# Kernel optimization log

Hardware: AMD Instinct MI355X
Metric: run time of the kernel (lower is better)

## Reference

```python
import jax, jax.numpy as jnp
import numpy as np

NUM_MID = 10   # hard-coded num_mid_nodes in HiPool.__init__
NUM_HIGH = 5   # ceil(10 / 2)


def map_low_to_high(num_low, num_high):
    # eye(num_high) repeat_interleaved by ceil(low/high) rows, truncated to num_low
    # == one-hot of i // edges_per_high
    edges_per_high = -(-num_low // num_high)
    return jax.nn.one_hot(jnp.arange(num_low) // edges_per_high, num_high,
                          dtype=jnp.float32)  # [low, high]


def cluster_attention(x, mapping, att):
    # x: [s, d], mapping: [s, m], att: [d, d]
    mid = mapping.T @ x                              # [m, d]
    scores = (mid @ att) @ x.T                       # [m, s]
    scores = scores * (1.0 - mapping).T              # zero (not -inf) own-cluster entries, as in source
    scores = jax.nn.softmax(scores, axis=1)
    return scores @ x + mid                          # [m, d]


def dense_gcn(x, adj, W, b):
    # torch_geometric DenseGCNConv with add_loop=True
    n = adj.shape[0]
    i = jnp.arange(n)
    adj = adj.at[i, i].set(1.0)
    deg = jnp.clip(jnp.sum(adj, axis=-1), 1.0, None) ** -0.5
    adj = deg[:, None] * adj * deg[None, :]
    return adj @ (x @ W) + b


def setup_inputs() -> dict:
    key = jax.random.key(0)
    ks = jax.random.split(key, 8)
    S, D, H = 8192, 768, 768
    return {
        "x": jax.random.normal(ks[0], (S, D), dtype=jnp.float32),
        "adjacency_matrix": jax.random.uniform(ks[1], (S, S), dtype=jnp.float32),
        "att_low_mid": jax.random.normal(ks[2], (D, D), dtype=jnp.float32) * 0.04,  # xavier_normal-ish
        "conv1_w": jax.random.normal(ks[3], (D, H), dtype=jnp.float32) * 0.04,
        "conv1_b": jnp.zeros((H,), dtype=jnp.float32),
        "att_mid_high": jax.random.normal(ks[4], (H, H), dtype=jnp.float32) * 0.04,
        "conv2_w": jax.random.normal(ks[5], (H, H), dtype=jnp.float32) * 0.04,
        "conv2_b": jnp.zeros((H,), dtype=jnp.float32),
    }


def reference(x, adjacency_matrix, att_low_mid, conv1_w, conv1_b,
              att_mid_high, conv2_w, conv2_b):
    s = x.shape[0]
    m1 = map_low_to_high(s, NUM_MID)                         # [s, 10]
    mid_adj = m1.T @ adjacency_matrix @ m1                   # [10, 10]
    mid_rep = cluster_attention(x, m1, att_low_mid)          # [10, d]
    x_mid = jax.nn.relu(dense_gcn(mid_rep, mid_adj, conv1_w, conv1_b))
    # F.dropout(...)[0]: dropout treated as identity (eval); [0] just dropped the batch dim
    m2 = map_low_to_high(NUM_MID, NUM_HIGH)                  # [10, 5]
    high_adj = m2.T @ mid_adj @ m2                           # [5, 5]
    high_rep = cluster_attention(x_mid, m2, att_mid_high)    # [5, h]
    out = jax.nn.relu(dense_gcn(high_rep, high_adj, conv2_w, conv2_b))
    return out.mean(axis=0)                                  # [h]
```

## Files before the change

### kernel.cpp

```cpp
#include <hip/hip_runtime.h>

constexpr int S    = 8192;
constexpr int D    = 768;
constexpr int NMID = 10;
constexpr int EPH  = 820;

constexpr int ADJ_SPLIT = 40;

constexpr int PART_ADJ = 0;
constexpr int PART_MID = 4096;
constexpr int OFF_Y1   = 65536;
constexpr int OFF_MATT = 73216;
constexpr int OFF_XMID = 80896;
constexpr int OFF_Z2   = 88576;
constexpr int OFF_SCB  = 92416;
constexpr int OFF_PVP  = 95232;

__device__ __forceinline__ void adj_item(const float* __restrict__ A,
                                         float* __restrict__ ws, int item) {
    __shared__ float bucket[2560];
    __shared__ float red2[160];
    int i = item / ADJ_SPLIT, s = item % ADJ_SPLIT;
    int r0 = i * EPH, nr = min(EPH, S - r0);
    int rs0 = r0 + nr * s / ADJ_SPLIT, rs1 = r0 + nr * (s + 1) / ADJ_SPLIT;
    int tid = threadIdx.x;
    float acc[8];
#pragma unroll
    for (int u = 0; u < 8; ++u) acc[u] = 0.f;
    for (int r = rs0; r < rs1; ++r) {
        const float4* row = (const float4*)(A + (size_t)r * S);
#pragma unroll
        for (int u = 0; u < 8; ++u) {
            float4 v = row[tid + 256 * u];
            acc[u] += (v.x + v.y) + (v.z + v.w);
        }
    }
    for (int t = tid; t < 2560; t += 256) bucket[t] = 0.f;
    __syncthreads();
#pragma unroll
    for (int u = 0; u < 8; ++u) {
        int j = ((tid + 256 * u) * 4) / 820;
        bucket[j * 256 + tid] += acc[u];
    }
    __syncthreads();
    if (tid < 160) {
        int j = tid >> 4, seg = tid & 15;
        float sm = 0.f;
#pragma unroll
        for (int u = 0; u < 16; ++u) sm += bucket[j * 256 + seg * 16 + u];
        red2[tid] = sm;
    }
    __syncthreads();
    if (tid < 10) {
        float sm = 0.f;
#pragma unroll
        for (int g = 0; g < 16; ++g) sm += red2[tid * 16 + g];
        ws[PART_ADJ + item * 10 + tid] = sm;
    }
}

__device__ __forceinline__ void mid_partial(const float* __restrict__ x,
                                            float* __restrict__ ws, int item) {
    int cl = item / 24, rem = item % 24;
    int cc = rem >> 3, sp = rem & 7;
    int r0 = cl * EPH, nr = min(EPH, S - r0);
    int rs0 = r0 + (nr * sp) / 8, rs1 = r0 + (nr * (sp + 1)) / 8;
    int c = cc * 256 + threadIdx.x;
    float acc = 0.f;
    for (int r = rs0; r < rs1; ++r) acc += x[(size_t)r * D + c];
    ws[PART_MID + (sp * NMID + cl) * D + c] = acc;
}

template <int NR>
__device__ __forceinline__ void mm_core(const float* __restrict__ W,
                                        const float* mi,
                                        float* __restrict__ out, int kb) {
    int c = threadIdx.x;
    float a0[NR], a1[NR], a2[NR];
#pragma unroll
    for (int i = 0; i < NR; ++i) { a0[i] = 0.f; a1[i] = 0.f; a2[i] = 0.f; }
    for (int kk = 0; kk < 16; ++kk) {
        const float* wr = W + (size_t)(kb + kk) * D;
        float w0 = wr[c], w1 = wr[c + 256], w2 = wr[c + 512];
#pragma unroll
        for (int i = 0; i < NR; ++i) {
            float m = mi[i * 16 + kk];
            a0[i] += m * w0; a1[i] += m * w1; a2[i] += m * w2;
        }
    }
#pragma unroll
    for (int i = 0; i < NR; ++i) {
        atomicAdd(&out[i * D + c],       a0[i]);
        atomicAdd(&out[i * D + c + 256], a1[i]);
        atomicAdd(&out[i * D + c + 512], a2[i]);
    }
}

template <int NR>
__device__ __forceinline__ void fullk_slice(const float* __restrict__ W,
                                            const float* inL, float* red,
                                            float* outS, int c0) {
    int tid = threadIdx.x;
    int c = tid & 15, ks = tid >> 4;
    float acc[NR];
#pragma unroll
    for (int i = 0; i < NR; ++i) acc[i] = 0.f;
    int kb = ks * 48;
    for (int kk = 0; kk < 48; ++kk) {
        int k = kb + kk;
        float w = W[(size_t)k * D + c0 + c];
#pragma unroll
        for (int i = 0; i < NR; ++i) acc[i] += inL[i * D + k] * w;
    }
#pragma unroll
    for (int i = 0; i < NR; ++i) red[(ks * NR + i) * 16 + c] = acc[i];
    __syncthreads();
    if (tid < NR * 16) {
        int i = tid >> 4, cc = tid & 15;
        float s = 0.f;
#pragma unroll
        for (int k2 = 0; k2 < 16; ++k2) s += red[(k2 * NR + i) * 16 + cc];
        outS[i * 16 + cc] = s;
    }
    __syncthreads();
}

__global__ __launch_bounds__(256) void k1(const float* __restrict__ A,
                                          const float* __restrict__ x,
                                          float* __restrict__ ws) {
    int bx = blockIdx.x;
    if (bx < 240) mid_partial(x, ws, bx);
    else if (bx < 500) adj_item(A, ws, bx - 240);
    else {
        int b = bx - 500;
        for (int t = b * 256 + threadIdx.x; t < 7680; t += 512)
            ws[OFF_Y1 + t] = 0.f;
    }
}

__global__ __launch_bounds__(256) void k2(const float* __restrict__ attL,
                                          const float* __restrict__ A,
                                          float* __restrict__ ws) {
    int bx = blockIdx.x, tid = threadIdx.x;
    if (bx >= 48) { adj_item(A, ws, 260 + bx - 48); return; }
    __shared__ float midL[7680];
    __shared__ float red[2560];
    __shared__ float outS[160];
    for (int t = tid; t < 7680; t += 256) {
        int cl = t / D, k = t - cl * D;
        float s = 0.f;
#pragma unroll
        for (int sp = 0; sp < 8; ++sp)
            s += ws[PART_MID + (sp * NMID + cl) * D + k];
        midL[t] = s;
    }
    __syncthreads();
    fullk_slice<10>(attL, midL, red, outS, bx * 16);
    if (tid < 160) ws[OFF_MATT + (tid >> 4) * D + bx * 16 + (tid & 15)] = outS[tid];
}

__global__ __launch_bounds__(256) void k3(const float* __restrict__ x,
                                          const float* __restrict__ A,
                                          float* __restrict__ ws) {
    int bx = blockIdx.x, tid = threadIdx.x;
    if (bx >= 128) { adj_item(A, ws, 330 + bx - 128); return; }
    __shared__ float ma[7680];
    __shared__ float sl[640];
    __shared__ float mloc[10];
    for (int t = tid; t < 7680; t += 256) ma[t] = ws[OFF_MATT + t];
    __syncthreads();
    const float4* maf = (const float4*)ma;
    const float4* x4  = (const float4*)x;
    int wave = tid >> 6, ln = tid & 63;
    int r0 = bx * 64;
    for (int rr = 0; rr < 16; ++rr) {
        int rl = wave * 16 + rr;
        int r = r0 + rl;
        float4 v0 = x4[(size_t)r * 192 + ln];
        float4 v1 = x4[(size_t)r * 192 + 64 + ln];
        float4 v2 = x4[(size_t)r * 192 + 128 + ln];
        int rc = r / EPH;
#pragma unroll
        for (int i = 0; i < NMID; ++i) {
            float4 m0 = maf[i * 192 + ln];
            float4 m1 = maf[i * 192 + 64 + ln];
            float4 m2 = maf[i * 192 + 128 + ln];
            float p = m0.x * v0.x + m0.y * v0.y + m0.z * v0.z + m0.w * v0.w
                    + m1.x * v1.x + m1.y * v1.y + m1.z * v1.z + m1.w * v1.w
                    + m2.x * v2.x + m2.y * v2.y + m2.z * v2.z + m2.w * v2.w;
#pragma unroll
            for (int off = 32; off > 0; off >>= 1) p += __shfl_down(p, off, 64);
            if (ln == 0) sl[rl * NMID + i] = (rc == i) ? 0.f : p;
        }
    }
    __syncthreads();
    if (tid < NMID) {
        float m = -1e30f;
        for (int r = 0; r < 64; ++r) m = fmaxf(m, sl[r * NMID + tid]);
        float s = 0.f;
        for (int r = 0; r < 64; ++r) s += expf(sl[r * NMID + tid] - m);
        mloc[tid] = m;
        ws[OFF_SCB + bx * 20 + tid * 2]     = m;
        ws[OFF_SCB + bx * 20 + tid * 2 + 1] = s;
    }
    __syncthreads();
    for (int t = tid; t < 640; t += 256) sl[t] = expf(sl[t] - mloc[t % NMID]);
    __syncthreads();
    float a0[NMID], a1[NMID], a2[NMID];
#pragma unroll
    for (int i = 0; i < NMID; ++i) { a0[i] = 0.f; a1[i] = 0.f; a2[i] = 0.f; }
    for (int r = 0; r < 64; ++r) {
        const float* xr = x + (size_t)(r0 + r) * D;
        float x0 = xr[tid], x1 = xr[tid + 256], x2 = xr[tid + 512];
#pragma unroll
        for (int i = 0; i < NMID; ++i) {
            float w = sl[r * NMID + i];
            a0[i] += w * x0; a1[i] += w * x1; a2[i] += w * x2;
        }
    }
#pragma unroll
    for (int i = 0; i < NMID; ++i) {
        float* base = ws + OFF_PVP + (bx * NMID + i) * D;
        base[tid]       = a0[i];
        base[tid + 256] = a1[i];
        base[tid + 512] = a2[i];
    }
}

__global__ __launch_bounds__(256) void k4(const float* __restrict__ W1,
                                          float* __restrict__ ws) {
    __shared__ float lm[160], ls[160], Mi[16], Zi[16];
    __shared__ float wts[1280];
    __shared__ float mi[160];
    int tid = threadIdx.x, kb = blockIdx.x * 16;
    if (tid < 160) {
        int i = tid >> 4, seg = tid & 15;
        float m = -1e30f;
        for (int b = seg * 8; b < seg * 8 + 8; ++b)
            m = fmaxf(m, ws[OFF_SCB + b * 20 + i * 2]);
        float s = 0.f;
        for (int b = seg * 8; b < seg * 8 + 8; ++b)
            s += ws[OFF_SCB + b * 20 + i * 2 + 1] *
                 expf(ws[OFF_SCB + b * 20 + i * 2] - m);
        lm[tid] = m; ls[tid] = s;
    }
    __syncthreads();
    if (tid < NMID) {
        float M = -1e30f;
        for (int g = 0; g < 16; ++g) M = fmaxf(M, lm[tid * 16 + g]);
        float Z = 0.f;
        for (int g = 0; g < 16; ++g) Z += ls[tid * 16 + g] * expf(lm[tid * 16 + g] - M);
        Mi[tid] = M; Zi[tid] = 1.f / Z;
    }
    __syncthreads();
    for (int t = tid; t < 1280; t += 256) {
        int b = t / NMID, i = t % NMID;
        wts[t] = expf(ws[OFF_SCB + b * 20 + i * 2] - Mi[i]) * Zi[i];
    }
    __syncthreads();
    if (tid < 160) {
        int i = tid >> 4, k = kb + (tid & 15);
        float s = 0.f;
#pragma unroll
        for (int sp = 0; sp < 8; ++sp)
            s += ws[PART_MID + (sp * NMID + i) * D + k];
        for (int b = 0; b < 128; ++b)
            s += wts[b * NMID + i] * ws[OFF_PVP + (b * NMID + i) * D + k];
        mi[tid] = s;
    }
    __syncthreads();
    mm_core<10>(W1, mi, ws + OFF_Y1, kb);
}

__global__ __launch_bounds__(256) void k5(const float* __restrict__ attH,
                                          const float* __restrict__ b1,
                                          float* __restrict__ ws) {
    __shared__ float xmidL[7680];
    __shared__ float mid2L[3840];
    __shared__ float red[1280];
    __shared__ float z2s[80];
    __shared__ float aa[100], dg[16], NM[100];
    int tid = threadIdx.x, kb = blockIdx.x * 16;

    if (tid < 100) {
        int i = tid / 10, j = tid % 10;
        float s = 0.f;
        for (int sp = 0; sp < ADJ_SPLIT; ++sp)
            s += ws[PART_ADJ + (i * ADJ_SPLIT + sp) * 10 + j];
        aa[tid] = s;
    }
    __syncthreads();
    if (tid < 10) {
        float s = 0.f;
#pragma unroll
        for (int j = 0; j < 10; ++j) s += (tid == j) ? 1.f : aa[tid * 10 + j];
        dg[tid] = 1.f / sqrtf(fmaxf(s, 1.f));
    }
    __syncthreads();
    if (tid < 100) {
        int i = tid / 10, j = tid % 10;
        NM[tid] = dg[i] * ((i == j) ? 1.f : aa[tid]) * dg[j];
    }
    __syncthreads();
    for (int c = tid; c < D; c += 256) {
        float yv[10];
#pragma unroll
        for (int j = 0; j < 10; ++j) yv[j] = ws[OFF_Y1 + j * D + c];
        float bias = b1[c];
        float xm[10];
#pragma unroll
        for (int i = 0; i < 10; ++i) {
            float v = bias;
#pragma unroll
            for (int j = 0; j < 10; ++j) v += NM[i * 10 + j] * yv[j];
            xm[i] = fmaxf(v, 0.f);
            xmidL[i * D + c] = xm[i];
        }
#pragma unroll
        for (int a = 0; a < 5; ++a)
            mid2L[a * D + c] = xm[2 * a] + xm[2 * a + 1];
    }
    __syncthreads();
    if (tid < 160) {
        int i = tid >> 4, cc = tid & 15;
        ws[OFF_XMID + i * D + kb + cc] = xmidL[i * D + kb + cc];
    }
    fullk_slice<5>(attH, mid2L, red, z2s, kb);
    if (tid < 80) ws[OFF_Z2 + (tid >> 4) * D + kb + (tid & 15)] = z2s[tid];
}

__global__ __launch_bounds__(256) void k6(const float* __restrict__ W2,
                                          const float* __restrict__ b2,
                                          float* __restrict__ ws,
                                          float* __restrict__ out) {
    __shared__ float xmidL[7680];
    __shared__ float out2L[3840];
    __shared__ float red[1280];
    __shared__ float Y2s[80];
    __shared__ float sred[200], s2l[64], P2[50];
    __shared__ float aa[100], ha[32], dh[8], NH[32];
    int tid = threadIdx.x, kb = blockIdx.x * 16;

    for (int t = tid; t < 7680; t += 256) xmidL[t] = ws[OFF_XMID + t];
    if (tid >= 56 && tid < 156) {
        int t2 = tid - 56;
        int i = t2 / 10, j = t2 % 10;
        float s = 0.f;
        for (int sp = 0; sp < ADJ_SPLIT; ++sp)
            s += ws[PART_ADJ + (i * ADJ_SPLIT + sp) * 10 + j];
        aa[t2] = s;
    }
    __syncthreads();
    if (tid < 200) {
        int pp = tid >> 2, q = tid & 3;
        int i = pp / 10, r = pp % 10;
        const float* z = ws + OFF_Z2 + i * D;
        float s = 0.f;
        for (int c = q * 192; c < q * 192 + 192; ++c)
            s += z[c] * xmidL[r * D + c];
        sred[tid] = s;
    }
    __syncthreads();
    if (tid < 50) {
        int i = tid / 10, r = tid % 10;
        float v = sred[tid * 4] + sred[tid * 4 + 1] + sred[tid * 4 + 2] + sred[tid * 4 + 3];
        s2l[tid] = ((r >> 1) == i) ? 0.f : v;
    }
    __syncthreads();
    if (tid < 5) {
        float mx = -1e30f;
#pragma unroll
        for (int r = 0; r < 10; ++r) mx = fmaxf(mx, s2l[tid * 10 + r]);
        float sm = 0.f; float e[10];
#pragma unroll
        for (int r = 0; r < 10; ++r) { e[r] = expf(s2l[tid * 10 + r] - mx); sm += e[r]; }
#pragma unroll
        for (int r = 0; r < 10; ++r) P2[tid * 10 + r] = e[r] / sm;
    }
    __syncthreads();
    for (int t = tid; t < 3840; t += 256) {
        int i = t / D, k = t - i * D;
        float v = xmidL[(2 * i) * D + k] + xmidL[(2 * i + 1) * D + k];
#pragma unroll
        for (int r = 0; r < 10; ++r) v += P2[i * 10 + r] * xmidL[r * D + k];
        out2L[t] = v;
    }
    __syncthreads();
    fullk_slice<5>(W2, out2L, red, Y2s, kb);
    if (tid < 25) {
        int a = tid / 5, b = tid % 5;
        ha[tid] = aa[(2 * a) * 10 + 2 * b] + aa[(2 * a) * 10 + 2 * b + 1]
                + aa[(2 * a + 1) * 10 + 2 * b] + aa[(2 * a + 1) * 10 + 2 * b + 1];
    }
    __syncthreads();
    if (tid < 5) {
        float s = 0.f;
#pragma unroll
        for (int j = 0; j < 5; ++j) s += (tid == j) ? 1.f : ha[tid * 5 + j];
        dh[tid] = 1.f / sqrtf(fmaxf(s, 1.f));
    }
    __syncthreads();
    if (tid < 25) {
        int i = tid / 5, j = tid % 5;
        NH[tid] = dh[i] * ((i == j) ? 1.f : ha[tid]) * dh[j];
    }
    __syncthreads();
    if (tid < 16) {
        int c = kb + tid;
        float bias = b2[c];
        float s = 0.f;
#pragma unroll
        for (int i = 0; i < 5; ++i) {
            float v = bias;
#pragma unroll
            for (int j = 0; j < 5; ++j) v += NH[i * 5 + j] * Y2s[j * 16 + tid];
            s += fmaxf(v, 0.f);
        }
        out[c] = s * 0.2f;
    }
}

extern "C" void kernel_launch(void* const* d_in, const int* in_sizes, int n_in,
                              void* d_out, int out_size, void* d_ws, size_t ws_size,
                              hipStream_t stream) {
    const float* x    = (const float*)d_in[0];
    const float* adj  = (const float*)d_in[1];
    const float* attL = (const float*)d_in[2];
    const float* W1   = (const float*)d_in[3];
    const float* b1   = (const float*)d_in[4];
    const float* attH = (const float*)d_in[5];
    const float* W2   = (const float*)d_in[6];
    const float* b2   = (const float*)d_in[7];
    float* ws  = (float*)d_ws;
    float* out = (float*)d_out;

    k1<<<502, 256, 0, stream>>>(adj, x, ws);
    k2<<<118, 256, 0, stream>>>(attL, adj, ws);
    k3<<<198, 256, 0, stream>>>(x, adj, ws);
    k4<<<48,  256, 0, stream>>>(W1, ws);
    k5<<<48,  256, 0, stream>>>(attH, b1, ws);
    k6<<<48,  256, 0, stream>>>(W2, b2, ws, out);
}
```

Baseline: 162.4 us.

## Move adjacency reduction into one wide first kernel, pre-reduce partials

The 256 MB adjacency row/column-bucket reduction was previously spread over 400 large work items (each roughly 20 rows) piggybacked on k1, k2 and k3. It now runs entirely in k1 across 2048 small blocks of 4 rows each, giving far more parallelism for the bandwidth-bound pass. k2 and k3 become plain compute kernels, so they lose the overlap with adjacency streaming they had before. Two extra blocks in k4 pre-reduce the 2048 partials into the 10x10 matrix once, so k5 and k6 just load it.

```diff
diff --git a/kernel.cpp b/kernel.cpp
--- a/kernel.cpp
+++ b/kernel.cpp
@@ -5,59 +5,17 @@
 constexpr int NMID = 10;
 constexpr int EPH  = 820;
 
-constexpr int ADJ_SPLIT = 40;
+constexpr int ADJ_BLKS = 2048;
 
 constexpr int PART_ADJ = 0;
-constexpr int PART_MID = 4096;
-constexpr int OFF_Y1   = 65536;
-constexpr int OFF_MATT = 73216;
-constexpr int OFF_XMID = 80896;
-constexpr int OFF_Z2   = 88576;
-constexpr int OFF_SCB  = 92416;
-constexpr int OFF_PVP  = 95232;
-
-__device__ __forceinline__ void adj_item(const float* __restrict__ A,
-                                         float* __restrict__ ws, int item) {
-    __shared__ float bucket[2560];
-    __shared__ float red2[160];
-    int i = item / ADJ_SPLIT, s = item % ADJ_SPLIT;
-    int r0 = i * EPH, nr = min(EPH, S - r0);
-    int rs0 = r0 + nr * s / ADJ_SPLIT, rs1 = r0 + nr * (s + 1) / ADJ_SPLIT;
-    int tid = threadIdx.x;
-    float acc[8];
-#pragma unroll
-    for (int u = 0; u < 8; ++u) acc[u] = 0.f;
-    for (int r = rs0; r < rs1; ++r) {
-        const float4* row = (const float4*)(A + (size_t)r * S);
-#pragma unroll
-        for (int u = 0; u < 8; ++u) {
-            float4 v = row[tid + 256 * u];
-            acc[u] += (v.x + v.y) + (v.z + v.w);
-        }
-    }
-    for (int t = tid; t < 2560; t += 256) bucket[t] = 0.f;
-    __syncthreads();
-#pragma unroll
-    for (int u = 0; u < 8; ++u) {
-        int j = ((tid + 256 * u) * 4) / 820;
-        bucket[j * 256 + tid] += acc[u];
-    }
-    __syncthreads();
-    if (tid < 160) {
-        int j = tid >> 4, seg = tid & 15;
-        float sm = 0.f;
-#pragma unroll
-        for (int u = 0; u < 16; ++u) sm += bucket[j * 256 + seg * 16 + u];
-        red2[tid] = sm;
-    }
-    __syncthreads();
-    if (tid < 10) {
-        float sm = 0.f;
-#pragma unroll
-        for (int g = 0; g < 16; ++g) sm += red2[tid * 16 + g];
-        ws[PART_ADJ + item * 10 + tid] = sm;
-    }
-}
+constexpr int PART_MID = 20480;
+constexpr int OFF_AA   = 81920;
+constexpr int OFF_Y1   = 82048;
+constexpr int OFF_MATT = 89728;
+constexpr int OFF_XMID = 97408;
+constexpr int OFF_Z2   = 105088;
+constexpr int OFF_SCB  = 108928;
+constexpr int OFF_PVP  = 111616;
 
 __device__ __forceinline__ void mid_partial(const float* __restrict__ x,
                                             float* __restrict__ ws, int item) {
@@ -128,24 +86,59 @@
 __global__ __launch_bounds__(256) void k1(const float* __restrict__ A,
                                           const float* __restrict__ x,
                                           float* __restrict__ ws) {
-    int bx = blockIdx.x;
-    if (bx < 240) mid_partial(x, ws, bx);
-    else if (bx < 500) adj_item(A, ws, bx - 240);
-    else {
-        int b = bx - 500;
-        for (int t = b * 256 + threadIdx.x; t < 7680; t += 512)
+    int bx = blockIdx.x, tid = threadIdx.x;
+    if (bx < ADJ_BLKS) {
+        __shared__ float bucket[2560];
+        __shared__ float red2[160];
+        int r0 = bx * 4;
+        float acc[8];
+#pragma unroll
+        for (int u = 0; u < 8; ++u) acc[u] = 0.f;
+        for (int r = r0; r < r0 + 4; ++r) {
+            const float4* row = (const float4*)(A + (size_t)r * S);
+#pragma unroll
+            for (int u = 0; u < 8; ++u) {
+                float4 v = row[tid + 256 * u];
+                acc[u] += (v.x + v.y) + (v.z + v.w);
+            }
+        }
+        for (int t = tid; t < 2560; t += 256) bucket[t] = 0.f;
+        __syncthreads();
+#pragma unroll
+        for (int u = 0; u < 8; ++u) {
+            int j = (tid + 256 * u) / 205;
+            bucket[j * 256 + tid] += acc[u];
+        }
+        __syncthreads();
+        if (tid < 160) {
+            int j = tid >> 4, seg = tid & 15;
+            float sm = 0.f;
+#pragma unroll
+            for (int u = 0; u < 16; ++u) sm += bucket[j * 256 + seg * 16 + u];
+            red2[tid] = sm;
+        }
+        __syncthreads();
+        if (tid < 10) {
+            float sm = 0.f;
+#pragma unroll
+            for (int g = 0; g < 16; ++g) sm += red2[tid * 16 + g];
+            ws[PART_ADJ + bx * 10 + tid] = sm;
+        }
+    } else if (bx < ADJ_BLKS + 240) {
+        mid_partial(x, ws, bx - ADJ_BLKS);
+    } else {
+        int b = bx - (ADJ_BLKS + 240);
+        for (int t = b * 256 + tid; t < 7680; t += 512)
             ws[OFF_Y1 + t] = 0.f;
     }
 }
 
 __global__ __launch_bounds__(256) void k2(const float* __restrict__ attL,
-                                          const float* __restrict__ A,
                                           float* __restrict__ ws) {
-    int bx = blockIdx.x, tid = threadIdx.x;
-    if (bx >= 48) { adj_item(A, ws, 260 + bx - 48); return; }
     __shared__ float midL[7680];
     __shared__ float red[2560];
     __shared__ float outS[160];
+    int tid = threadIdx.x, bx = blockIdx.x;
     for (int t = tid; t < 7680; t += 256) {
         int cl = t / D, k = t - cl * D;
         float s = 0.f;
@@ -160,13 +153,11 @@
 }
 
 __global__ __launch_bounds__(256) void k3(const float* __restrict__ x,
-                                          const float* __restrict__ A,
                                           float* __restrict__ ws) {
-    int bx = blockIdx.x, tid = threadIdx.x;
-    if (bx >= 128) { adj_item(A, ws, 330 + bx - 128); return; }
     __shared__ float ma[7680];
     __shared__ float sl[640];
     __shared__ float mloc[10];
+    int tid = threadIdx.x, bx = blockIdx.x;
     for (int t = tid; t < 7680; t += 256) ma[t] = ws[OFF_MATT + t];
     __syncthreads();
     const float4* maf = (const float4*)ma;
@@ -229,10 +220,29 @@
 
 __global__ __launch_bounds__(256) void k4(const float* __restrict__ W1,
                                           float* __restrict__ ws) {
+    int tid = threadIdx.x, bx = blockIdx.x;
+    if (bx >= 48) {
+        __shared__ float ared[256];
+        int base = (bx - 48) * 50;
+        float s = 0.f;
+        if (tid < 200) {
+            int p = base + (tid >> 2), q = tid & 3;
+            int i = p / 10, j = p % 10;
+            int b0 = i * 205 + q * 52;
+            int b1 = i * 205 + min((q + 1) * 52, 205);
+            for (int b = b0; b < b1; ++b) s += ws[PART_ADJ + b * 10 + j];
+        }
+        if (tid < 256) ared[tid] = s;
+        __syncthreads();
+        if (tid < 50)
+            ws[OFF_AA + base + tid] = ared[tid * 4] + ared[tid * 4 + 1]
+                                    + ared[tid * 4 + 2] + ared[tid * 4 + 3];
+        return;
+    }
     __shared__ float lm[160], ls[160], Mi[16], Zi[16];
     __shared__ float wts[1280];
     __shared__ float mi[160];
-    int tid = threadIdx.x, kb = blockIdx.x * 16;
+    int kb = bx * 16;
     if (tid < 160) {
         int i = tid >> 4, seg = tid & 15;
         float m = -1e30f;
@@ -282,13 +292,7 @@
     __shared__ float aa[100], dg[16], NM[100];
     int tid = threadIdx.x, kb = blockIdx.x * 16;
 
-    if (tid < 100) {
-        int i = tid / 10, j = tid % 10;
-        float s = 0.f;
-        for (int sp = 0; sp < ADJ_SPLIT; ++sp)
-            s += ws[PART_ADJ + (i * ADJ_SPLIT + sp) * 10 + j];
-        aa[tid] = s;
-    }
+    if (tid < 100) aa[tid] = ws[OFF_AA + tid];
     __syncthreads();
     if (tid < 10) {
         float s = 0.f;
@@ -342,14 +346,7 @@
     int tid = threadIdx.x, kb = blockIdx.x * 16;
 
     for (int t = tid; t < 7680; t += 256) xmidL[t] = ws[OFF_XMID + t];
-    if (tid >= 56 && tid < 156) {
-        int t2 = tid - 56;
-        int i = t2 / 10, j = t2 % 10;
-        float s = 0.f;
-        for (int sp = 0; sp < ADJ_SPLIT; ++sp)
-            s += ws[PART_ADJ + (i * ADJ_SPLIT + sp) * 10 + j];
-        aa[t2] = s;
-    }
+    if (tid >= 56 && tid < 156) aa[tid - 56] = ws[OFF_AA + tid - 56];
     __syncthreads();
     if (tid < 200) {
         int pp = tid >> 2, q = tid & 3;
@@ -434,10 +431,10 @@
     float* ws  = (float*)d_ws;
     float* out = (float*)d_out;
 
-    k1<<<502, 256, 0, stream>>>(adj, x, ws);
-    k2<<<118, 256, 0, stream>>>(attL, adj, ws);
-    k3<<<198, 256, 0, stream>>>(x, adj, ws);
-    k4<<<48,  256, 0, stream>>>(W1, ws);
+    k1<<<ADJ_BLKS + 240 + 2, 256, 0, stream>>>(adj, x, ws);
+    k2<<<48,  256, 0, stream>>>(attL, ws);
+    k3<<<128, 256, 0, stream>>>(x, ws);
+    k4<<<50,  256, 0, stream>>>(W1, ws);
     k5<<<48,  256, 0, stream>>>(attH, b1, ws);
     k6<<<48,  256, 0, stream>>>(W2, b2, ws, out);
 }
```

Result: slower. 180.3 us (+11.0%).
